# Performance work log

Measured on AMD Instinct MI355X. Metric: run time of the kernel, lower is better.

## Reference

```python
import jax, jax.numpy as jnp
import numpy as np

H = 1024      # hidden_dim
NH = 16       # num_heads
HD = H // NH  # head_dim
FFN = 4096
EPS = 1e-5


def setup_inputs() -> dict:
    key = jax.random.key(0)
    ks = jax.random.split(key, 12)
    s = 0.02
    return {
        "x": jax.random.normal(ks[0], (2, 2048, H), dtype=jnp.float32),
        "w_qkv": jax.random.normal(ks[1], (H, 3 * H), dtype=jnp.float32) * s,
        "b_qkv": jnp.zeros((3 * H,), dtype=jnp.float32),
        "w_out": jax.random.normal(ks[2], (H, H), dtype=jnp.float32) * s,
        "b_out": jnp.zeros((H,), dtype=jnp.float32),
        "ln1_g": jnp.ones((H,), dtype=jnp.float32),
        "ln1_b": jnp.zeros((H,), dtype=jnp.float32),
        "ln2_g": jnp.ones((H,), dtype=jnp.float32),
        "ln2_b": jnp.zeros((H,), dtype=jnp.float32),
        "w1": jax.random.normal(ks[3], (H, FFN), dtype=jnp.float32) * s,
        "b1": jnp.zeros((FFN,), dtype=jnp.float32),
        "w2": jax.random.normal(ks[4], (FFN, H), dtype=jnp.float32) * s,
        "b2": jnp.zeros((H,), dtype=jnp.float32),
    }


def _layernorm(x, g, b):
    mu = jnp.mean(x, axis=-1, keepdims=True)
    var = jnp.mean(jnp.square(x - mu), axis=-1, keepdims=True)
    return (x - mu) * jax.lax.rsqrt(var + EPS) * g + b


def reference(x, w_qkv, b_qkv, w_out, b_out, ln1_g, ln1_b, ln2_g, ln2_b, w1, b1, w2, b2):
    B, S, _ = x.shape
    # pre-LN attention branch
    h = _layernorm(x, ln1_g, ln1_b)
    qkv = h @ w_qkv + b_qkv                       # (B,S,3H)
    qkv = qkv.reshape(B, S, 3, NH, HD).transpose(2, 0, 3, 1, 4)
    q, k, v = qkv[0], qkv[1], qkv[2]              # (B,NH,S,HD)
    scores = jnp.einsum("bhqd,bhkd->bhqk", q, k) / jnp.sqrt(jnp.float32(HD))
    causal = jnp.triu(jnp.ones((S, S), dtype=bool), k=1)
    scores = jnp.where(causal, -jnp.inf, scores)
    attn = jax.nn.softmax(scores, axis=-1)
    out = jnp.einsum("bhqk,bhkd->bhqd", attn, v)  # (B,NH,S,HD)
    out = out.transpose(0, 2, 1, 3).reshape(B, S, H)
    attn_out = out @ w_out + b_out
    x = x + attn_out
    # FFN branch
    h2 = _layernorm(x, ln2_g, ln2_b)
    ffn = jax.nn.gelu(h2 @ w1 + b1, approximate=False) @ w2 + b2
    return x + ffn
```

## Files before the change

### kernel.cpp

```cpp
#include <hip/hip_runtime.h>
#include <hip/hip_bf16.h>

typedef __bf16 bf16_t;
typedef __bf16 bf16x8 __attribute__((ext_vector_type(8)));
typedef __bf16 bf16x4 __attribute__((ext_vector_type(4)));
typedef __bf16 bf16x2 __attribute__((ext_vector_type(2)));
typedef float  f32x4  __attribute__((ext_vector_type(4)));

#define HDIM 1024
#define SEQ  2048
#define NHEAD 16
#define HEADD 64

__device__ __forceinline__ void gld_lds16(const void* g, void* l) {
  __builtin_amdgcn_global_load_lds(
      (const __attribute__((address_space(1))) unsigned int*)g,
      (__attribute__((address_space(3))) unsigned int*)l, 16, 0, 0);
}

__global__ __launch_bounds__(256) void ln_kernel(const float* __restrict__ x,
                                                 const float* __restrict__ gam,
                                                 const float* __restrict__ bet,
                                                 bf16_t* __restrict__ out) {
  int row = blockIdx.x;
  int t = threadIdx.x;
  const float4* xr = (const float4*)(x + (size_t)row * HDIM);
  float4 v = xr[t];
  float s = v.x + v.y + v.z + v.w;
  float ss = v.x*v.x + v.y*v.y + v.z*v.z + v.w*v.w;
  #pragma unroll
  for (int o = 32; o > 0; o >>= 1) {
    s  += __shfl_xor(s, o);
    ss += __shfl_xor(ss, o);
  }
  __shared__ float red[8];
  int w = t >> 6;
  if ((t & 63) == 0) { red[w*2] = s; red[w*2+1] = ss; }
  __syncthreads();
  s  = red[0] + red[2] + red[4] + red[6];
  ss = red[1] + red[3] + red[5] + red[7];
  float mu  = s * (1.0f / HDIM);
  float var = ss * (1.0f / HDIM) - mu * mu;
  float rstd = rsqrtf(var + 1e-5f);
  float4 g4 = ((const float4*)gam)[t];
  float4 b4 = ((const float4*)bet)[t];
  bf16x4 o4;
  o4[0] = (bf16_t)((v.x - mu) * rstd * g4.x + b4.x);
  o4[1] = (bf16_t)((v.y - mu) * rstd * g4.y + b4.y);
  o4[2] = (bf16_t)((v.z - mu) * rstd * g4.z + b4.z);
  o4[3] = (bf16_t)((v.w - mu) * rstd * g4.w + b4.w);
  *(bf16x4*)(out + (size_t)row * HDIM + t * 4) = o4;
}

__global__ __launch_bounds__(256) void transpose_cast(const float* __restrict__ W,
                                                      bf16_t* __restrict__ Wt,
                                                      int Kd, int Nd) {
  __shared__ float tile[32][33];
  int n0 = blockIdx.x * 32, k0 = blockIdx.y * 32;
  int tx = threadIdx.x & 31, ty = threadIdx.x >> 5;
  #pragma unroll
  for (int i = 0; i < 4; i++)
    tile[ty + i*8][tx] = W[(size_t)(k0 + ty + i*8) * Nd + n0 + tx];
  __syncthreads();
  #pragma unroll
  for (int i = 0; i < 4; i++)
    Wt[(size_t)(n0 + ty + i*8) * Kd + k0 + tx] = (bf16_t)tile[tx][ty + i*8];
}

__device__ __forceinline__ float gelu_fast(float x) {
  float y = 0.7978845608f * (x + 0.044715f * x * x * x);
  float u = exp2f(y * 2.885390082f);
  float th = 1.0f - 2.0f * __builtin_amdgcn_rcpf(u + 1.0f);
  return 0.5f * x * (1.0f + th);
}

__global__ __launch_bounds__(256)
void reduce2_kernel(const bf16_t* __restrict__ p0, const bf16_t* __restrict__ p1,
                    const float* __restrict__ bias, const float* __restrict__ resid,
                    float* __restrict__ out) {
  size_t base = ((size_t)blockIdx.x * 256 + threadIdx.x) * 8;
  bf16x8 a = *(const bf16x8*)(p0 + base);
  bf16x8 b = *(const bf16x8*)(p1 + base);
  int col = (int)(base & (HDIM - 1));
  float4 bi0 = *(const float4*)(bias + col);
  float4 bi1 = *(const float4*)(bias + col + 4);
  float4 r0 = *(const float4*)(resid + base);
  float4 r1 = *(const float4*)(resid + base + 4);
  float4 o0, o1;
  o0.x = (float)a[0] + (float)b[0] + bi0.x + r0.x;
  o0.y = (float)a[1] + (float)b[1] + bi0.y + r0.y;
  o0.z = (float)a[2] + (float)b[2] + bi0.z + r0.z;
  o0.w = (float)a[3] + (float)b[3] + bi0.w + r0.w;
  o1.x = (float)a[4] + (float)b[4] + bi1.x + r1.x;
  o1.y = (float)a[5] + (float)b[5] + bi1.y + r1.y;
  o1.z = (float)a[6] + (float)b[6] + bi1.z + r1.z;
  o1.w = (float)a[7] + (float)b[7] + bi1.w + r1.w;
  *(float4*)(out + base)     = o0;
  *(float4*)(out + base + 4) = o1;
}

template<int EPI, int BN, int SPLITK>
__global__ __launch_bounds__(256, 2)
void gemm_bt(const bf16_t* __restrict__ A, const bf16_t* __restrict__ Bt,
             const float* __restrict__ bias, const float* __restrict__ resid,
             void* __restrict__ outp, int M, int N, int K) {
  constexpr int NFRAG = BN / 32;
  __shared__ bf16_t As[2][128*64];
  __shared__ bf16_t Bs[2][BN*64];
  int t = threadIdx.x;
  int w = t >> 6, l = t & 63;
  int wr = w >> 1, wc = w & 1;

  int nbx = gridDim.x;
  int bid = blockIdx.y * nbx + blockIdx.x;
  int chunkx = (nbx * gridDim.y) >> 3;
  int nb = (bid & 7) * chunkx + (bid >> 3);
  int bm = nb / nbx, bn = nb % nbx;
  size_t m0 = (size_t)bm * 128, n0 = (size_t)bn * BN;

  const int KK = (SPLITK > 1) ? K / SPLITK : K;
  const size_t koff = (SPLITK > 1) ? (size_t)blockIdx.z * KK : 0;

  f32x4 acc[4][NFRAG];
  #pragma unroll
  for (int m = 0; m < 4; m++)
    #pragma unroll
    for (int n = 0; n < NFRAG; n++) acc[m][n] = (f32x4)(0.0f);

  int srow = t >> 3;
  int scol = ((t & 7) ^ (srow & 7)) * 8;
  int dsto = t * 8;
  const bf16_t* ag = A  + (m0 + srow) * K + koff + scol;
  const bf16_t* bg = Bt + (n0 + srow) * K + koff + scol;

  int lr = l & 15, lg = l >> 4;

  auto stage = [&](int buf, int k0) {
    #pragma unroll
    for (int p = 0; p < 4; p++)
      gld_lds16(ag + k0 + (size_t)(p*32)*K, &As[buf][dsto + p*32*64]);
    #pragma unroll
    for (int p = 0; p < BN/32; p++)
      gld_lds16(bg + k0 + (size_t)(p*32)*K, &Bs[buf][dsto + p*32*64]);
  };

  stage(0, 0);
  __syncthreads();
  int cur = 0;
  const int NK = KK / 64;
  for (int k = 0; k < NK; k++) {
    if (k + 1 < NK) stage(cur ^ 1, (k + 1) * 64);
    #pragma unroll
    for (int kk = 0; kk < 2; kk++) {
      bf16x8 af[4], bfr[NFRAG];
      #pragma unroll
      for (int m = 0; m < 4; m++) {
        int row = wr*64 + m*16 + lr;
        int off = row*128 + (((kk*4 + lg) ^ (row & 7)) << 4);
        af[m] = *(const bf16x8*)((const char*)&As[cur][0] + off);
      }
      #pragma unroll
      for (int n = 0; n < NFRAG; n++) {
        int row = wc*(BN/2) + n*16 + lr;
        int off = row*128 + (((kk*4 + lg) ^ (row & 7)) << 4);
        bfr[n] = *(const bf16x8*)((const char*)&Bs[cur][0] + off);
      }
      #pragma unroll
      for (int m = 0; m < 4; m++)
        #pragma unroll
        for (int n = 0; n < NFRAG; n++)
          acc[m][n] = __builtin_amdgcn_mfma_f32_16x16x32_bf16(af[m], bfr[n], acc[m][n], 0, 0, 0);
    }
    __syncthreads();
    cur ^= 1;
  }

  int r0 = (l >> 4) * 4, c0 = l & 15;
  bf16_t* pd = nullptr;
  if (EPI == 3)
    pd = (bf16_t*)(blockIdx.z == 0 ? outp : (void*)resid);
  #pragma unroll
  for (int m = 0; m < 4; m++) {
    #pragma unroll
    for (int n = 0; n < NFRAG; n++) {
      size_t row = m0 + wr*64 + m*16 + r0;
      size_t col = n0 + wc*(BN/2) + n*16 + c0;
      float bv = (EPI == 3) ? 0.0f : bias[col];
      #pragma unroll
      for (int r = 0; r < 4; r++) {
        float vv = acc[m][n][r] + bv;
        size_t idx = (row + r) * (size_t)N + col;
        if (EPI == 0) {
          ((bf16_t*)outp)[idx] = (bf16_t)vv;
        } else if (EPI == 1) {
          ((float*)outp)[idx] = vv + resid[idx];
        } else if (EPI == 2) {
          ((bf16_t*)outp)[idx] = (bf16_t)gelu_fast(vv);
        } else {
          pd[idx] = (bf16_t)vv;
        }
      }
    }
  }
}

__global__ __launch_bounds__(512, 4)
void attn_kernel(const bf16_t* __restrict__ qkv, bf16_t* __restrict__ out) {
  int idx = blockIdx.x;
  int half = idx >> 8;
  int sub = idx & 255;
  int qth = sub >> 5;
  int qt = half ? qth : (15 - qth);
  int bh = sub & 31;
  int b = bh >> 4, h = bh & 15;
  int t = threadIdx.x, w = t >> 6, l = t & 63;

  __shared__ bf16_t Ks[2][64*64];
  __shared__ bf16_t Vt[2][64*72];
  __shared__ bf16_t Ps[8][16*64];

  const size_t RS = 3 * HDIM;
  const bf16_t* qb = qkv + (size_t)b * SEQ * RS + h * HEADD;
  const bf16_t* kb = qb + HDIM;
  const bf16_t* vb = qb + 2 * HDIM;

  int lr = l & 15, lg = l >> 4;
  const float SCALE = 0.125f * 1.44269504f;

  bf16x8 qf[2];
  {
    size_t qrow = (size_t)qt * 128 + w * 16 + lr;
    qf[0] = *(const bf16x8*)(qb + qrow * RS + lg * 8);
    qf[1] = *(const bf16x8*)(qb + qrow * RS + 32 + lg * 8);
    #pragma unroll
    for (int i = 0; i < 8; i++) {
      qf[0][i] = (bf16_t)((float)qf[0][i] * SCALE);
      qf[1][i] = (bf16_t)((float)qf[1][i] * SCALE);
    }
  }

  f32x4 o[4];
  #pragma unroll
  for (int d = 0; d < 4; d++) o[d] = (f32x4)(0.0f);
  float m = -1e30f, lsum = 0.0f;

  int srow = t >> 3, scol = (t & 7) * 8;
  int Fv = ((scol >> 3) & 7) << 3;
  int nkt = 2 * qt + 2;

  const bf16_t* kg0 = kb + (size_t)srow * RS + scol;
  const bf16_t* vg0 = vb + (size_t)srow * RS + scol;

  bf16x8 kr = *(const bf16x8*)kg0;
  bf16x8 vr = *(const bf16x8*)vg0;

  int wrow0 = qt * 128 + w * 16;
  int qg = wrow0 + lr;
  bf16_t* pw = Ps[w];
  int psw = (lr & 7) << 4;
  int cur = 0;

  for (int kt = 0; kt < nkt; kt++) {
    {
      int ba = srow * 128 + scol * 2;
      int sw = (srow & 7) << 4;
      *(bf16x8*)((char*)Ks[cur] + (ba ^ sw)) = kr;
      int ksw = srow ^ Fv;
      bf16_t* vt = Vt[cur];
      #pragma unroll
      for (int i = 0; i < 8; i++)
        vt[(scol + i) * 72 + ksw] = vr[i];
    }
    if (kt + 1 < nkt) {
      kr = *(const bf16x8*)(kg0 + (size_t)(kt + 1) * 64 * RS);
      vr = *(const bf16x8*)(vg0 + (size_t)(kt + 1) * 64 * RS);
    }
    __syncthreads();

    bool skipw = (kt * 64) > (wrow0 + 15);
    if (!skipw) {
      f32x4 sc[4];
      #pragma unroll
      for (int kt2 = 0; kt2 < 4; kt2++) {
        sc[kt2] = (f32x4)(0.0f);
        #pragma unroll
        for (int kk = 0; kk < 2; kk++) {
          int row = kt2 * 16 + lr;
          int off = (row * 128 + kk * 64 + lg * 16) ^ ((row & 7) << 4);
          bf16x8 kf = *(const bf16x8*)((char*)Ks[cur] + off);
          sc[kt2] = __builtin_amdgcn_mfma_f32_16x16x32_bf16(kf, qf[kk], sc[kt2], 0, 0, 0);
        }
      }
      if (kt * 64 + 63 > wrow0) {
        #pragma unroll
        for (int kt2 = 0; kt2 < 4; kt2++) {
          #pragma unroll
          for (int r = 0; r < 4; r++) {
            int kcol = kt*64 + kt2*16 + lg*4 + r;
            if (kcol > qg) sc[kt2][r] = -1e30f;
          }
        }
      }
      float tm0 = fmaxf(fmaxf(sc[0][0], sc[0][1]), fmaxf(sc[0][2], sc[0][3]));
      float tm1 = fmaxf(fmaxf(sc[1][0], sc[1][1]), fmaxf(sc[1][2], sc[1][3]));
      float tm2 = fmaxf(fmaxf(sc[2][0], sc[2][1]), fmaxf(sc[2][2], sc[2][3]));
      float tm3 = fmaxf(fmaxf(sc[3][0], sc[3][1]), fmaxf(sc[3][2], sc[3][3]));
      float tm = fmaxf(fmaxf(tm0, tm1), fmaxf(tm2, tm3));
      tm = fmaxf(tm, __shfl_xor(tm, 16));
      tm = fmaxf(tm, __shfl_xor(tm, 32));
      if (!__all(tm <= m + 8.0f)) {
        float nm = fmaxf(m, tm);
        float alpha = exp2f(m - nm);
        m = nm;
        lsum *= alpha;
        #pragma unroll
        for (int d = 0; d < 4; d++)
          #pragma unroll
          for (int r = 0; r < 4; r++) o[d][r] *= alpha;
      }
      #pragma unroll
      for (int kt2 = 0; kt2 < 4; kt2++) {
        float p0 = exp2f(sc[kt2][0] - m);
        float p1 = exp2f(sc[kt2][1] - m);
        float p2 = exp2f(sc[kt2][2] - m);
        float p3 = exp2f(sc[kt2][3] - m);
        lsum += (p0 + p1) + (p2 + p3);
        bf16x2 pa; pa[0] = (bf16_t)p0; pa[1] = (bf16_t)p1;
        bf16x2 pb; pb[0] = (bf16_t)p2; pb[1] = (bf16_t)p3;
        int base = lr * 128 + kt2 * 32 + lg * 8;
        *(bf16x2*)((char*)pw + ((base)     ^ psw)) = pa;
        *(bf16x2*)((char*)pw + ((base + 4) ^ psw)) = pb;
      }
      asm volatile("s_waitcnt lgkmcnt(0)" ::: "memory");
      #pragma unroll
      for (int kk = 0; kk < 2; kk++) {
        int poff = (lr * 128 + kk * 64 + lg * 16) ^ psw;
        bf16x8 pf = *(const bf16x8*)((char*)pw + poff);
        #pragma unroll
        for (int dblk = 0; dblk < 4; dblk++) {
          int vrow = dblk * 16 + lr;
          int Fd = ((vrow >> 3) & 7) << 3;
          bf16x8 vf = *(const bf16x8*)(Vt[cur] + vrow * 72 + ((kk * 32 + lg * 8) ^ Fd));
          o[dblk] = __builtin_amdgcn_mfma_f32_16x16x32_bf16(vf, pf, o[dblk], 0, 0, 0);
        }
      }
    }
    cur ^= 1;
  }

  lsum += __shfl_xor(lsum, 16);
  lsum += __shfl_xor(lsum, 32);
  float inv = 1.0f / lsum;

  bf16_t* ob = out + ((size_t)b * SEQ + qg) * HDIM + h * HEADD;
  #pragma unroll
  for (int dblk = 0; dblk < 4; dblk++) {
    bf16x4 q4;
    #pragma unroll
    for (int r = 0; r < 4; r++) q4[r] = (bf16_t)(o[dblk][r] * inv);
    *(bf16x4*)(ob + dblk * 16 + lg * 4) = q4;
  }
}

extern "C" void kernel_launch(void* const* d_in, const int* in_sizes, int n_in,
                              void* d_out, int out_size, void* d_ws, size_t ws_size,
                              hipStream_t stream) {
  (void)in_sizes; (void)n_in; (void)out_size; (void)ws_size;
  const float* x     = (const float*)d_in[0];
  const float* w_qkv = (const float*)d_in[1];
  const float* b_qkv = (const float*)d_in[2];
  const float* w_out = (const float*)d_in[3];
  const float* b_out = (const float*)d_in[4];
  const float* ln1_g = (const float*)d_in[5];
  const float* ln1_b = (const float*)d_in[6];
  const float* ln2_g = (const float*)d_in[7];
  const float* ln2_b = (const float*)d_in[8];
  const float* w1    = (const float*)d_in[9];
  const float* b1    = (const float*)d_in[10];
  const float* w2    = (const float*)d_in[11];
  const float* b2    = (const float*)d_in[12];
  float* out = (float*)d_out;

  char* ws = (char*)d_ws;
  size_t off = 0;
  auto alloc = [&](size_t bytes) -> void* {
    void* p = ws + off;
    off += (bytes + 255) & ~(size_t)255;
    return p;
  };
  bf16_t* wqkvT = (bf16_t*)alloc((size_t)3072*1024*2);
  bf16_t* woutT = (bf16_t*)alloc((size_t)1024*1024*2);
  bf16_t* w1T   = (bf16_t*)alloc((size_t)4096*1024*2);
  bf16_t* w2T   = (bf16_t*)alloc((size_t)1024*4096*2);
  bf16_t* ln1o  = (bf16_t*)alloc((size_t)4096*1024*2);
  bf16_t* qkvb  = (bf16_t*)alloc((size_t)4096*4096*2);
  bf16_t* attno = (bf16_t*)alloc((size_t)4096*1024*2);
  float*  x2    = (float*) alloc((size_t)4096*1024*4);
  bf16_t* h2 = ln1o;
  bf16_t* g  = qkvb;
  bf16_t* part0 = ln1o;
  bf16_t* part1 = attno;

  dim3 blk(256);
  transpose_cast<<<dim3(3072/32, 1024/32), blk, 0, stream>>>(w_qkv, wqkvT, 1024, 3072);
  transpose_cast<<<dim3(1024/32, 1024/32), blk, 0, stream>>>(w_out, woutT, 1024, 1024);
  transpose_cast<<<dim3(4096/32, 1024/32), blk, 0, stream>>>(w1,    w1T,   1024, 4096);
  transpose_cast<<<dim3(1024/32, 4096/32), blk, 0, stream>>>(w2,    w2T,   4096, 1024);

  ln_kernel<<<4096, blk, 0, stream>>>(x, ln1_g, ln1_b, ln1o);
  gemm_bt<0,128,1><<<dim3(24, 32), blk, 0, stream>>>(ln1o, wqkvT, b_qkv, nullptr, qkvb, 4096, 3072, 1024);
  attn_kernel<<<512, dim3(512), 0, stream>>>(qkvb, attno);
  gemm_bt<1,64,1><<<dim3(16, 32), blk, 0, stream>>>(attno, woutT, b_out, x, x2, 4096, 1024, 1024);
  ln_kernel<<<4096, blk, 0, stream>>>(x2, ln2_g, ln2_b, h2);
  gemm_bt<2,128,1><<<dim3(32, 32), blk, 0, stream>>>(h2, w1T, b1, nullptr, g, 4096, 4096, 1024);
  gemm_bt<3,128,2><<<dim3(8, 32, 2), blk, 0, stream>>>(g, w2T, b2, (const float*)part1, part0, 4096, 1024, 4096);
  reduce2_kernel<<<2048, blk, 0, stream>>>(part0, part1, b2, x2, out);
}
```

Before: 231.2 us.

## Add 256x256-tile 4-stage pipelined GEMM for QKV and FFN1, set MFMA priority

Adds a new 512-thread GEMM kernel with 256x256 output tiles, a 4-buffer global-to-LDS pipeline using direct LDS loads, and XOR-swizzled LDS reads. It replaces the 128-wide gemm_bt for the QKV projection and the first FFN matmul. The aim is more data reuse per tile and better latency hiding. It also wraps the MFMA sections in the attention kernel with s_setprio so matrix issue gets priority. The cost is a much smaller grid (192 and 256 blocks), which can leave CUs underused. It also raises register and LDS pressure.

```diff
diff --git a/kernel.cpp b/kernel.cpp
--- a/kernel.cpp
+++ b/kernel.cpp
@@ -99,6 +99,101 @@
   *(float4*)(out + base + 4) = o1;
 }
 
+template<int EPI>
+__global__ __launch_bounds__(512, 2)
+void gemm256(const bf16_t* __restrict__ A, const bf16_t* __restrict__ Bt,
+             const float* __restrict__ bias, void* __restrict__ outp,
+             int M, int N, int K) {
+  __shared__ bf16_t As[4][256*32];
+  __shared__ bf16_t Bs[4][256*32];
+  int t = threadIdx.x;
+  int wid = t >> 6, l = t & 63;
+  int wm = wid >> 2, wn = wid & 3;
+
+  int nbx = gridDim.x;
+  int bid = blockIdx.y * nbx + blockIdx.x;
+  int chunkx = (nbx * gridDim.y) >> 3;
+  int nb = (bid & 7) * chunkx + (bid >> 3);
+  int bm = nb / nbx, bn = nb % nbx;
+  size_t m0 = (size_t)bm * 256, n0 = (size_t)bn * 256;
+
+  f32x4 acc[8][4];
+  #pragma unroll
+  for (int m = 0; m < 8; m++)
+    #pragma unroll
+    for (int n = 0; n < 4; n++) acc[m][n] = (f32x4)(0.0f);
+
+  int srow = t >> 2;
+  int scol = ((t & 3) ^ ((srow >> 1) & 3)) * 8;
+  int dsto = t * 8;
+  const bf16_t* ag = A  + (m0 + srow) * K + scol;
+  const bf16_t* bg = Bt + (n0 + srow) * K + scol;
+  int lr = l & 15, lg = l >> 4;
+
+  auto stage = [&](int buf, int kt) {
+    int k0 = kt * 32;
+    gld_lds16(ag + k0, &As[buf][dsto]);
+    gld_lds16(ag + k0 + (size_t)128 * K, &As[buf][dsto + 128*32]);
+    gld_lds16(bg + k0, &Bs[buf][dsto]);
+    gld_lds16(bg + k0 + (size_t)128 * K, &Bs[buf][dsto + 128*32]);
+  };
+
+  const int NK = K / 32;
+  stage(0, 0); stage(1, 1); stage(2, 2);
+  asm volatile("s_waitcnt vmcnt(8)" ::: "memory");
+  __builtin_amdgcn_s_barrier();
+  __builtin_amdgcn_sched_barrier(0);
+
+  for (int k = 0; k < NK; k++) {
+    int buf = k & 3;
+    if (k + 3 < NK) stage((k + 3) & 3, k + 3);
+    bf16x8 af[8], bfr[4];
+    #pragma unroll
+    for (int m = 0; m < 8; m++) {
+      int row = wm*128 + m*16 + lr;
+      int off = row*64 + ((lg ^ ((row >> 1) & 3)) << 4);
+      af[m] = *(const bf16x8*)((const char*)&As[buf][0] + off);
+    }
+    #pragma unroll
+    for (int n = 0; n < 4; n++) {
+      int row = wn*64 + n*16 + lr;
+      int off = row*64 + ((lg ^ ((row >> 1) & 3)) << 4);
+      bfr[n] = *(const bf16x8*)((const char*)&Bs[buf][0] + off);
+    }
+    __builtin_amdgcn_s_setprio(1);
+    #pragma unroll
+    for (int m = 0; m < 8; m++)
+      #pragma unroll
+      for (int n = 0; n < 4; n++)
+        acc[m][n] = __builtin_amdgcn_mfma_f32_16x16x32_bf16(af[m], bfr[n], acc[m][n], 0, 0, 0);
+    __builtin_amdgcn_s_setprio(0);
+    if (k < NK - 1) {
+      if (k + 3 < NK)      asm volatile("s_waitcnt vmcnt(8)" ::: "memory");
+      else if (k + 2 < NK) asm volatile("s_waitcnt vmcnt(4)" ::: "memory");
+      else                 asm volatile("s_waitcnt vmcnt(0)" ::: "memory");
+      __builtin_amdgcn_s_barrier();
+      __builtin_amdgcn_sched_barrier(0);
+    }
+  }
+
+  #pragma unroll
+  for (int m = 0; m < 8; m++) {
+    #pragma unroll
+    for (int n = 0; n < 4; n++) {
+      size_t row = m0 + wm*128 + m*16 + lg*4;
+      size_t col = n0 + wn*64 + n*16 + lr;
+      float bv = bias[col];
+      #pragma unroll
+      for (int r = 0; r < 4; r++) {
+        float vv = acc[m][n][r] + bv;
+        size_t idx = (row + r) * (size_t)N + col;
+        if (EPI == 0) ((bf16_t*)outp)[idx] = (bf16_t)vv;
+        else          ((bf16_t*)outp)[idx] = (bf16_t)gelu_fast(vv);
+      }
+    }
+  }
+}
+
 template<int EPI, int BN, int SPLITK>
 __global__ __launch_bounds__(256, 2)
 void gemm_bt(const bf16_t* __restrict__ A, const bf16_t* __restrict__ Bt,
@@ -190,15 +285,8 @@
       for (int r = 0; r < 4; r++) {
         float vv = acc[m][n][r] + bv;
         size_t idx = (row + r) * (size_t)N + col;
-        if (EPI == 0) {
-          ((bf16_t*)outp)[idx] = (bf16_t)vv;
-        } else if (EPI == 1) {
-          ((float*)outp)[idx] = vv + resid[idx];
-        } else if (EPI == 2) {
-          ((bf16_t*)outp)[idx] = (bf16_t)gelu_fast(vv);
-        } else {
-          pd[idx] = (bf16_t)vv;
-        }
+        if (EPI == 1)      ((float*)outp)[idx] = vv + resid[idx];
+        else if (EPI == 3) pd[idx] = (bf16_t)vv;
       }
     }
   }
@@ -280,6 +368,7 @@
     bool skipw = (kt * 64) > (wrow0 + 15);
     if (!skipw) {
       f32x4 sc[4];
+      __builtin_amdgcn_s_setprio(1);
       #pragma unroll
       for (int kt2 = 0; kt2 < 4; kt2++) {
         sc[kt2] = (f32x4)(0.0f);
@@ -291,6 +380,7 @@
           sc[kt2] = __builtin_amdgcn_mfma_f32_16x16x32_bf16(kf, qf[kk], sc[kt2], 0, 0, 0);
         }
       }
+      __builtin_amdgcn_s_setprio(0);
       if (kt * 64 + 63 > wrow0) {
         #pragma unroll
         for (int kt2 = 0; kt2 < 4; kt2++) {
@@ -332,6 +422,7 @@
         *(bf16x2*)((char*)pw + ((base + 4) ^ psw)) = pb;
       }
       asm volatile("s_waitcnt lgkmcnt(0)" ::: "memory");
+      __builtin_amdgcn_s_setprio(1);
       #pragma unroll
       for (int kk = 0; kk < 2; kk++) {
         int poff = (lr * 128 + kk * 64 + lg * 16) ^ psw;
@@ -344,6 +435,7 @@
           o[dblk] = __builtin_amdgcn_mfma_f32_16x16x32_bf16(vf, pf, o[dblk], 0, 0, 0);
         }
       }
+      __builtin_amdgcn_s_setprio(0);
     }
     cur ^= 1;
   }
@@ -408,11 +500,11 @@
   transpose_cast<<<dim3(1024/32, 4096/32), blk, 0, stream>>>(w2,    w2T,   4096, 1024);
 
   ln_kernel<<<4096, blk, 0, stream>>>(x, ln1_g, ln1_b, ln1o);
-  gemm_bt<0,128,1><<<dim3(24, 32), blk, 0, stream>>>(ln1o, wqkvT, b_qkv, nullptr, qkvb, 4096, 3072, 1024);
+  gemm256<0><<<dim3(12, 16), dim3(512), 0, stream>>>(ln1o, wqkvT, b_qkv, qkvb, 4096, 3072, 1024);
   attn_kernel<<<512, dim3(512), 0, stream>>>(qkvb, attno);
   gemm_bt<1,64,1><<<dim3(16, 32), blk, 0, stream>>>(attno, woutT, b_out, x, x2, 4096, 1024, 1024);
   ln_kernel<<<4096, blk, 0, stream>>>(x2, ln2_g, ln2_b, h2);
-  gemm_bt<2,128,1><<<dim3(32, 32), blk, 0, stream>>>(h2, w1T, b1, nullptr, g, 4096, 4096, 1024);
+  gemm256<2><<<dim3(16, 16), dim3(512), 0, stream>>>(h2, w1T, b1, g, 4096, 4096, 1024);
   gemm_bt<3,128,2><<<dim3(8, 32, 2), blk, 0, stream>>>(g, w2T, b2, (const float*)part1, part0, 4096, 1024, 4096);
   reduce2_kernel<<<2048, blk, 0, stream>>>(part0, part1, b2, x2, out);
 }
```

Measured after the change: 236.4 us. +2.3%, slower.
